# Performance work log

Measured on AMD Instinct MI355X. Metric: run time of the kernel, lower is better.

Reference implementation:

```python
import jax, jax.numpy as jnp
import numpy as np

B, L, D = 2, 2048, 2048
H, KVH = 16, 4
DK = D // H            # 128
REP = H // KVH         # 4
CAP = 50.0


def _rope(x):
    # x: [B, h, L, DK]; rotate-half style RoPE matching the torch module
    half = DK // 2
    inv_freq = 1.0 / (10000.0 ** (jnp.arange(0, DK, 2, dtype=jnp.float32) / DK))
    pos = jnp.arange(x.shape[2], dtype=jnp.float32)
    freqs = pos[:, None] * inv_freq[None, :]          # [L, DK/2]
    cos = jnp.cos(freqs).astype(x.dtype)
    sin = jnp.sin(freqs).astype(x.dtype)
    x1, x2 = x[..., :half], x[..., half:]
    return jnp.concatenate([x1 * cos - x2 * sin, x1 * sin + x2 * cos], axis=-1)


def setup_inputs() -> dict:
    key = jax.random.key(0)
    ks = jax.random.split(key, 7)
    query = jax.random.normal(ks[0], (B, L, D), jnp.float32)
    key_t = jax.random.normal(ks[1], (B, L, D), jnp.float32)
    value = jax.random.normal(ks[2], (B, L, D), jnp.float32)
    mask = jnp.tril(jnp.ones((L, L), dtype=bool))[None, None]  # causal, broadcast over B,H
    s = 1.0 / np.sqrt(D)
    Wq = jax.random.normal(ks[3], (D, D), jnp.float32) * s
    Wk = jax.random.normal(ks[4], (D // REP, D), jnp.float32) * s
    Wv = jax.random.normal(ks[5], (D // REP, D), jnp.float32) * s
    Wo = jax.random.normal(ks[6], (D, D), jnp.float32) * s
    return {"query": query, "key_t": key_t, "value": value, "mask": mask,
            "Wq": Wq, "Wk": Wk, "Wv": Wv, "Wo": Wo}


def reference(query, key_t, value, mask, Wq, Wk, Wv, Wo):
    Lk = key_t.shape[1]
    Q = (query @ Wq.T).reshape(B, L, H, DK).transpose(0, 2, 1, 3)        # [B,H,L,DK]
    K = (key_t @ Wk.T).reshape(B, Lk, KVH, DK).transpose(0, 2, 1, 3)     # [B,KVH,Lk,DK]
    V = (value @ Wv.T).reshape(B, Lk, KVH, DK).transpose(0, 2, 1, 3)
    # repeat_interleave KV heads to match query heads (GQA)
    K = jnp.repeat(K, REP, axis=1)
    V = jnp.repeat(V, REP, axis=1)
    Q = _rope(Q)
    K = _rope(K)
    # module implements "softcap" as a clamp on q/k pre-SDPA
    Q = jnp.clip(Q, -CAP, CAP)
    K = jnp.clip(K, -CAP, CAP)
    scale = 1.0 / np.sqrt(DK)  # SDPA default scaling
    logits = jnp.einsum('bhld,bhkd->bhlk', Q, K) * scale
    neg = jnp.finfo(logits.dtype).min
    logits = logits + jnp.where(mask, jnp.zeros((), logits.dtype), neg)
    attn = jax.nn.softmax(logits, axis=-1)
    out = jnp.einsum('bhlk,bhkd->bhld', attn, V)                         # [B,H,L,DK]
    out = out.transpose(0, 2, 1, 3).reshape(B, L, D)
    return out @ Wo.T
```

## Files before the change

### kernel.cpp

```cpp
#include <hip/hip_runtime.h>

typedef __bf16 bf16;
typedef __bf16 bf16x8 __attribute__((ext_vector_type(8)));
typedef float  f32x4  __attribute__((ext_vector_type(4)));

#define MFMA16(a, b, c) __builtin_amdgcn_mfma_f32_16x16x32_bf16((a), (b), (c), 0, 0, 0)

__device__ inline void gl_lds16(const bf16* g, bf16* l) {
  __builtin_amdgcn_global_load_lds(
      (const __attribute__((address_space(1))) void*)g,
      (__attribute__((address_space(3))) void*)l, 16, 0, 0);
}

__device__ inline bf16x8 cvt8(const float* __restrict__ f) {
  float4 a = *(const float4*)f;
  float4 b = *(const float4*)(f + 4);
  bf16x8 r;
  r[0] = (bf16)a.x; r[1] = (bf16)a.y; r[2] = (bf16)a.z; r[3] = (bf16)a.w;
  r[4] = (bf16)b.x; r[5] = (bf16)b.y; r[6] = (bf16)b.z; r[7] = (bf16)b.w;
  return r;
}

__global__ void cvt_f32_bf16(const float* __restrict__ src, bf16* __restrict__ dst,
                             int n8) {
  int i = blockIdx.x * 256 + threadIdx.x;
  if (i >= n8) return;
  *(bf16x8*)(dst + (size_t)i * 8) = cvt8(src + (size_t)i * 8);
}

__global__ __launch_bounds__(256) void gemm_qkv(const bf16* __restrict__ qA,
                                                const float* __restrict__ kA,
                                                const float* __restrict__ vA,
                                                const bf16* __restrict__ W,
                                                bf16* __restrict__ Qb,
                                                bf16* __restrict__ Kb,
                                                bf16* __restrict__ Vb) {
  __shared__ alignas(16) bf16 As[16 * 512];
  __shared__ alignas(16) bf16 Bs[16 * 512];

  const int tid  = threadIdx.x;
  const int wave = tid >> 6, lane = tid & 63;
  const int wm = wave >> 1, wn = wave & 1;
  const int lr = lane & 15, quad = lane >> 4;
  const int m0 = blockIdx.y * 128, n0 = blockIdx.x * 128;
  const int K = 2048;

  const int range = (n0 < 2048) ? 0 : (n0 < 2560) ? 1 : 2;
  const float* Af = (range == 1) ? kA : vA;

  f32x4 vzero = {0.f, 0.f, 0.f, 0.f};
  f32x4 acc[4][4];
#pragma unroll
  for (int mt = 0; mt < 4; ++mt)
#pragma unroll
    for (int nt = 0; nt < 4; ++nt) acc[mt][nt] = vzero;

  for (int k0 = 0; k0 < K; k0 += 64) {
#pragma unroll
    for (int j = 0; j < 4; ++j) {
      int c = wave * 4 + j;
      gl_lds16(W + (size_t)(n0 + (c >> 1) * 16 + lr) * K + k0 + (c & 1) * 32 + quad * 8,
               Bs + c * 512);
    }
    if (range == 0) {
#pragma unroll
      for (int j = 0; j < 4; ++j) {
        int c = wave * 4 + j;
        gl_lds16(qA + (size_t)(m0 + (c >> 1) * 16 + lr) * K +
                     k0 + (c & 1) * 32 + quad * 8,
                 As + c * 512);
      }
    } else {
#pragma unroll
      for (int j = 0; j < 4; ++j) {
        int c = wave * 4 + j;
        *(bf16x8*)(As + c * 512 + lane * 8) =
            cvt8(Af + (size_t)(m0 + (c >> 1) * 16 + lr) * K +
                 k0 + (c & 1) * 32 + quad * 8);
      }
    }
    __syncthreads();

#pragma unroll
    for (int s = 0; s < 2; ++s) {
      bf16x8 af[4], bfg[4];
#pragma unroll
      for (int mt = 0; mt < 4; ++mt)
        af[mt] = *(const bf16x8*)(As + ((wm * 4 + mt) * 2 + s) * 512 + lane * 8);
#pragma unroll
      for (int nt = 0; nt < 4; ++nt)
        bfg[nt] = *(const bf16x8*)(Bs + ((wn * 4 + nt) * 2 + s) * 512 + lane * 8);
#pragma unroll
      for (int mt = 0; mt < 4; ++mt)
#pragma unroll
        for (int nt = 0; nt < 4; ++nt)
          acc[mt][nt] = MFMA16(af[mt], bfg[nt], acc[mt][nt]);
    }
    __syncthreads();
  }

  bf16* Cb = (range == 0) ? Qb : (range == 1) ? Kb : Vb;
  const int ld = (range == 0) ? 2048 : 512;
  const int nb = (range == 0) ? n0 : (range == 1) ? n0 - 2048 : n0 - 2560;
#pragma unroll
  for (int mt = 0; mt < 4; ++mt) {
    int row = m0 + wm * 64 + mt * 16 + quad * 4;
#pragma unroll
    for (int nt = 0; nt < 4; ++nt) {
      int col = nb + wn * 64 + nt * 16 + lr;
#pragma unroll
      for (int e = 0; e < 4; ++e)
        Cb[(size_t)(row + e) * ld + col] = (bf16)acc[mt][nt][e];
    }
  }
}

template <bool OUTF32>
__global__ __launch_bounds__(256) void gemm_bt(const bf16* __restrict__ Ap,
                                               const bf16* __restrict__ W,
                                               void* __restrict__ C0,
                                               int ld0, int M, int N, int K) {
  __shared__ alignas(16) bf16 As[16 * 512];
  __shared__ alignas(16) bf16 Bs[16 * 512];

  const int tid  = threadIdx.x;
  const int wave = tid >> 6, lane = tid & 63;
  const int wm = wave >> 1, wn = wave & 1;
  const int lr = lane & 15, quad = lane >> 4;
  const int m0 = blockIdx.y * 128, n0 = blockIdx.x * 128;

  f32x4 vzero = {0.f, 0.f, 0.f, 0.f};
  f32x4 acc[4][4];
#pragma unroll
  for (int mt = 0; mt < 4; ++mt)
#pragma unroll
    for (int nt = 0; nt < 4; ++nt) acc[mt][nt] = vzero;

  for (int k0 = 0; k0 < K; k0 += 64) {
#pragma unroll
    for (int j = 0; j < 4; ++j) {
      int c = wave * 4 + j;
      gl_lds16(W + (size_t)(n0 + (c >> 1) * 16 + lr) * K + k0 + (c & 1) * 32 + quad * 8,
               Bs + c * 512);
      gl_lds16(Ap + (size_t)(m0 + (c >> 1) * 16 + lr) * K + k0 + (c & 1) * 32 + quad * 8,
               As + c * 512);
    }
    __syncthreads();

#pragma unroll
    for (int s = 0; s < 2; ++s) {
      bf16x8 af[4], bfg[4];
#pragma unroll
      for (int mt = 0; mt < 4; ++mt)
        af[mt] = *(const bf16x8*)(As + ((wm * 4 + mt) * 2 + s) * 512 + lane * 8);
#pragma unroll
      for (int nt = 0; nt < 4; ++nt)
        bfg[nt] = *(const bf16x8*)(Bs + ((wn * 4 + nt) * 2 + s) * 512 + lane * 8);
#pragma unroll
      for (int mt = 0; mt < 4; ++mt)
#pragma unroll
        for (int nt = 0; nt < 4; ++nt)
          acc[mt][nt] = MFMA16(af[mt], bfg[nt], acc[mt][nt]);
    }
    __syncthreads();
  }

#pragma unroll
  for (int mt = 0; mt < 4; ++mt) {
    int row = m0 + wm * 64 + mt * 16 + quad * 4;
#pragma unroll
    for (int nt = 0; nt < 4; ++nt) {
      int col = n0 + wn * 64 + nt * 16 + lr;
#pragma unroll
      for (int e = 0; e < 4; ++e) {
        if (OUTF32)
          ((float*)C0)[(size_t)(row + e) * ld0 + col] = acc[mt][nt][e];
        else
          ((bf16*)C0)[(size_t)(row + e) * ld0 + col] = (bf16)acc[mt][nt][e];
      }
    }
  }
}

__global__ void rope_clip(bf16* __restrict__ X, int heads, float scl) {
  int tpr = heads * 8;
  int idx = blockIdx.x * 256 + threadIdx.x;
  if (idx >= 4096 * tpr) return;
  int r = idx / tpr;
  int rem = idx - r * tpr;
  int h = rem >> 3, j0 = (rem & 7) * 8;
  int l = r & 2047;
  size_t base = (size_t)r * (heads * 128) + h * 128 + j0;
  bf16x8 x1 = *(const bf16x8*)(X + base);
  bf16x8 x2 = *(const bf16x8*)(X + base + 64);
  bf16x8 y1, y2;
#pragma unroll
  for (int t = 0; t < 8; ++t) {
    int j = j0 + t;
    float inv = expf(-(float)j * (9.210340371976184f / 64.0f));
    float s, c;
    sincosf((float)l * inv, &s, &c);
    float a = (float)x1[t], b = (float)x2[t];
    float u = a * c - b * s;
    float v = a * s + b * c;
    y1[t] = (bf16)(fminf(fmaxf(u, -50.f), 50.f) * scl);
    y2[t] = (bf16)(fminf(fmaxf(v, -50.f), 50.f) * scl);
  }
  *(bf16x8*)(X + base)      = y1;
  *(bf16x8*)(X + base + 64) = y2;
}

__global__ void transpose_bf16(const bf16* __restrict__ in, bf16* __restrict__ out,
                               int R, int Cc) {
  __shared__ bf16 t[32][33];
  int b = blockIdx.z;
  const bf16* ip = in + (size_t)b * R * Cc;
  bf16* op = out + (size_t)b * R * Cc;
  int c0 = blockIdx.x * 32, r0 = blockIdx.y * 32;
  int lx = threadIdx.x, ly = threadIdx.y;
#pragma unroll
  for (int i = 0; i < 32; i += 8)
    t[ly + i][lx] = ip[(size_t)(r0 + ly + i) * Cc + c0 + lx];
  __syncthreads();
#pragma unroll
  for (int i = 0; i < 32; i += 8)
    op[(size_t)(c0 + ly + i) * R + r0 + lx] = t[lx][ly + i];
}

__global__ __launch_bounds__(512, 2) void flash(const bf16* __restrict__ Q,
                                                const bf16* __restrict__ Kp,
                                                const bf16* __restrict__ Vt,
                                                bf16* __restrict__ Ctx) {
  __shared__ alignas(16) bf16 Ks[2][16 * 512];
  __shared__ alignas(16) bf16 Vs[2][16 * 512];
  __shared__ alignas(16) bf16 Ps[8][32 * 72];

  const int tid  = threadIdx.x;
  const int wave = tid >> 6, lane = tid & 63;
  const int lr = lane & 15, quad = lane >> 4;
  const int bh = blockIdx.y;
  const int b = bh >> 4, h = bh & 15, hk = h >> 2;
  const int p = blockIdx.x;
  const int qA0 = p * 128, qB0 = (15 - p) * 128;
  const int qbA = qA0 + wave * 16;
  const int qbB = qB0 + wave * 16;
  const int nt = (qB0 + 128) >> 6;

  bf16x8 qfA[4], qfB[4];
  {
    const bf16* qa = Q + ((size_t)(b * 2048 + qbA + lr)) * 2048 + h * 128 + quad * 8;
    const bf16* qbp = Q + ((size_t)(b * 2048 + qbB + lr)) * 2048 + h * 128 + quad * 8;
#pragma unroll
    for (int ks = 0; ks < 4; ++ks) {
      qfA[ks] = *(const bf16x8*)(qa + ks * 32);
      qfB[ks] = *(const bf16x8*)(qbp + ks * 32);
    }
  }

  f32x4 vzero = {0.f, 0.f, 0.f, 0.f};
  f32x4 oA[8], oB[8];
#pragma unroll
  for (int dt = 0; dt < 8; ++dt) { oA[dt] = vzero; oB[dt] = vzero; }
  float flsA[4] = {0.f, 0.f, 0.f, 0.f};
  float flsB[4] = {0.f, 0.f, 0.f, 0.f};

  const bf16* kbase = Kp + (size_t)(b * 2048) * 512 + hk * 128;
  const bf16* vbase = Vt + ((size_t)(b * 512 + hk * 128)) * 2048;

#define STAGE(bufi, kk)                                                         \
  do {                                                                          \
    _Pragma("unroll") for (int j = 0; j < 4; ++j) {                             \
      int c = wave * 4 + j;                                                     \
      if (c < 16) {                                                             \
        gl_lds16(kbase + (size_t)((kk) + (c >> 2) * 16 + lr) * 512 +            \
                     (c & 3) * 32 + quad * 8,                                   \
                 &Ks[bufi][c * 512]);                                           \
      } else {                                                                  \
        int c2 = c - 16;                                                        \
        gl_lds16(vbase + (size_t)((c2 >> 1) * 16 + lr) * 2048 + (kk) +          \
                     (c2 & 1) * 32 + quad * 8,                                  \
                 &Vs[bufi][c2 * 512]);                                          \
      }                                                                         \
    }                                                                           \
  } while (0)

  STAGE(0, 0);
  int cur = 0;

  for (int t = 0; t < nt; ++t) {
    const int k0 = t * 64;
    if (t + 1 < nt) {
      STAGE(cur ^ 1, k0 + 64);
      asm volatile("s_waitcnt vmcnt(4)" ::: "memory");
    } else {
      asm volatile("s_waitcnt vmcnt(0)" ::: "memory");
    }
    __builtin_amdgcn_s_barrier();

    const bf16* ksb = Ks[cur];
    const bf16* vsb = Vs[cur];

    if (k0 <= qbA + 15) {
      f32x4 sA[4], sB[4];
#pragma unroll
      for (int kt = 0; kt < 4; ++kt) { sA[kt] = vzero; sB[kt] = vzero; }
#pragma unroll
      for (int ks = 0; ks < 4; ++ks) {
#pragma unroll
        for (int kt = 0; kt < 4; ++kt) {
          bf16x8 kf = *(const bf16x8*)(ksb + (kt * 4 + ks) * 512 + lane * 8);
          sA[kt] = MFMA16(qfA[ks], kf, sA[kt]);
          sB[kt] = MFMA16(qfB[ks], kf, sB[kt]);
        }
      }
      bf16* pwA = Ps[wave];
      bf16* pwB = Ps[wave] + 16 * 72;
#pragma unroll
      for (int kt = 0; kt < 4; ++kt) {
        int kid = k0 + kt * 16 + lr;
#pragma unroll
        for (int e = 0; e < 4; ++e) {
          int qr = quad * 4 + e;
          float pa = (kid <= qbA + qr) ? __expf(sA[kt][e]) : 0.f;
          float pb = __expf(sB[kt][e]);
          flsA[e] += pa;
          flsB[e] += pb;
          pwA[qr * 72 + kt * 16 + lr] = (bf16)pa;
          pwB[qr * 72 + kt * 16 + lr] = (bf16)pb;
        }
      }
#pragma unroll
      for (int ks2 = 0; ks2 < 2; ++ks2) {
        bf16x8 pfA = *(const bf16x8*)(pwA + (size_t)lr * 72 + ks2 * 32 + quad * 8);
        bf16x8 pfB = *(const bf16x8*)(pwB + (size_t)lr * 72 + ks2 * 32 + quad * 8);
#pragma unroll
        for (int dt = 0; dt < 8; ++dt) {
          bf16x8 vf = *(const bf16x8*)(vsb + (dt * 2 + ks2) * 512 + lane * 8);
          oA[dt] = MFMA16(pfA, vf, oA[dt]);
          oB[dt] = MFMA16(pfB, vf, oB[dt]);
        }
      }
    } else if (k0 <= qbB + 15) {
      f32x4 s[4];
#pragma unroll
      for (int kt = 0; kt < 4; ++kt) s[kt] = vzero;
#pragma unroll
      for (int ks = 0; ks < 4; ++ks) {
#pragma unroll
        for (int kt = 0; kt < 4; ++kt) {
          bf16x8 kf = *(const bf16x8*)(ksb + (kt * 4 + ks) * 512 + lane * 8);
          s[kt] = MFMA16(qfB[ks], kf, s[kt]);
        }
      }
      bf16* pwB = Ps[wave] + 16 * 72;
#pragma unroll
      for (int kt = 0; kt < 4; ++kt) {
        int kid = k0 + kt * 16 + lr;
#pragma unroll
        for (int e = 0; e < 4; ++e) {
          int qr = quad * 4 + e;
          float pb = (kid <= qbB + qr) ? __expf(s[kt][e]) : 0.f;
          flsB[e] += pb;
          pwB[qr * 72 + kt * 16 + lr] = (bf16)pb;
        }
      }
#pragma unroll
      for (int ks2 = 0; ks2 < 2; ++ks2) {
        bf16x8 pf = *(const bf16x8*)(pwB + (size_t)lr * 72 + ks2 * 32 + quad * 8);
#pragma unroll
        for (int dt = 0; dt < 8; ++dt) {
          bf16x8 vf = *(const bf16x8*)(vsb + (dt * 2 + ks2) * 512 + lane * 8);
          oB[dt] = MFMA16(pf, vf, oB[dt]);
        }
      }
    }
    __builtin_amdgcn_s_barrier();
    cur ^= 1;
  }
#undef STAGE

#pragma unroll
  for (int e = 0; e < 4; ++e) {
    float sa = flsA[e];
    sa += __shfl_xor(sa, 1);
    sa += __shfl_xor(sa, 2);
    sa += __shfl_xor(sa, 4);
    sa += __shfl_xor(sa, 8);
    flsA[e] = 1.0f / sa;
    float sb = flsB[e];
    sb += __shfl_xor(sb, 1);
    sb += __shfl_xor(sb, 2);
    sb += __shfl_xor(sb, 4);
    sb += __shfl_xor(sb, 8);
    flsB[e] = 1.0f / sb;
  }

  bf16* ca = Ctx + ((size_t)(b * 2048 + qbA + quad * 4)) * 2048 + h * 128 + lr;
  bf16* cb = Ctx + ((size_t)(b * 2048 + qbB + quad * 4)) * 2048 + h * 128 + lr;
#pragma unroll
  for (int dt = 0; dt < 8; ++dt)
#pragma unroll
    for (int e = 0; e < 4; ++e) {
      ca[(size_t)e * 2048 + dt * 16] = (bf16)(oA[dt][e] * flsA[e]);
      cb[(size_t)e * 2048 + dt * 16] = (bf16)(oB[dt][e] * flsB[e]);
    }
}

extern "C" void kernel_launch(void* const* d_in, const int* in_sizes, int n_in,
                              void* d_out, int out_size, void* d_ws, size_t ws_size,
                              hipStream_t stream) {
  (void)in_sizes; (void)n_in; (void)out_size; (void)ws_size;
  const float* query = (const float*)d_in[0];
  const float* key_t = (const float*)d_in[1];
  const float* value = (const float*)d_in[2];
  const float* Wq = (const float*)d_in[4];
  const float* Wk = (const float*)d_in[5];
  const float* Wv = (const float*)d_in[6];
  const float* Wo = (const float*)d_in[7];

  const size_t MB = 1024ull * 1024ull;
  char* ws  = (char*)d_ws;
  bf16* qbf = (bf16*)(ws);
  bf16* wqb = (bf16*)(ws + 16 * MB);
  bf16* wkb = (bf16*)(ws + 24 * MB);
  bf16* wvb = (bf16*)(ws + 26 * MB);
  bf16* wob = (bf16*)(ws + 28 * MB);
  bf16* Qb  = (bf16*)(ws + 36 * MB);
  bf16* Kb  = (bf16*)(ws + 52 * MB);
  bf16* Vb  = (bf16*)(ws + 56 * MB);
  bf16* Vtb = (bf16*)(ws + 60 * MB);
  bf16* Ctx = qbf;

  cvt_f32_bf16<<<4096, 256, 0, stream>>>(query, qbf, 1048576);
  cvt_f32_bf16<<<2048, 256, 0, stream>>>(Wq, wqb, 524288);
  cvt_f32_bf16<<<512, 256, 0, stream>>>(Wk, wkb, 131072);
  cvt_f32_bf16<<<512, 256, 0, stream>>>(Wv, wvb, 131072);
  cvt_f32_bf16<<<2048, 256, 0, stream>>>(Wo, wob, 524288);

  gemm_qkv<<<dim3(24, 32), 256, 0, stream>>>(qbf, key_t, value, wqb, Qb, Kb, Vb);

  rope_clip<<<2048, 256, 0, stream>>>(Qb, 16, 0.08838834764831845f);
  rope_clip<<<512, 256, 0, stream>>>(Kb, 4, 1.0f);

  transpose_bf16<<<dim3(16, 64, 2), dim3(32, 8), 0, stream>>>(Vb, Vtb, 2048, 512);

  flash<<<dim3(8, 32), 512, 0, stream>>>(Qb, Kb, Vtb, Ctx);

  gemm_bt<true><<<dim3(16, 32), 256, 0, stream>>>(
      Ctx, wob, (float*)d_out, 2048, 4096, 2048, 2048);
}
```

Measured before the change: 471.1 us.

## Double-buffer LDS tiles in QKV and output GEMMs to overlap loads with MFMA

```diff
diff --git a/kernel.cpp b/kernel.cpp
--- a/kernel.cpp
+++ b/kernel.cpp
@@ -21,6 +21,13 @@
   return r;
 }
 
+__device__ inline bf16x8 cvt8v(float4 a, float4 b) {
+  bf16x8 r;
+  r[0] = (bf16)a.x; r[1] = (bf16)a.y; r[2] = (bf16)a.z; r[3] = (bf16)a.w;
+  r[4] = (bf16)b.x; r[5] = (bf16)b.y; r[6] = (bf16)b.z; r[7] = (bf16)b.w;
+  return r;
+}
+
 __global__ void cvt_f32_bf16(const float* __restrict__ src, bf16* __restrict__ dst,
                              int n8) {
   int i = blockIdx.x * 256 + threadIdx.x;
@@ -35,15 +42,15 @@
                                                 bf16* __restrict__ Qb,
                                                 bf16* __restrict__ Kb,
                                                 bf16* __restrict__ Vb) {
-  __shared__ alignas(16) bf16 As[16 * 512];
-  __shared__ alignas(16) bf16 Bs[16 * 512];
+  __shared__ alignas(16) bf16 As[2][16 * 512];
+  __shared__ alignas(16) bf16 Bs[2][16 * 512];
 
   const int tid  = threadIdx.x;
   const int wave = tid >> 6, lane = tid & 63;
   const int wm = wave >> 1, wn = wave & 1;
   const int lr = lane & 15, quad = lane >> 4;
   const int m0 = blockIdx.y * 128, n0 = blockIdx.x * 128;
-  const int K = 2048;
+  const int NS = 32;
 
   const int range = (n0 < 2048) ? 0 : (n0 < 2560) ? 1 : 2;
   const float* Af = (range == 1) ? kA : vA;
@@ -55,49 +62,118 @@
 #pragma unroll
     for (int nt = 0; nt < 4; ++nt) acc[mt][nt] = vzero;
 
-  for (int k0 = 0; k0 < K; k0 += 64) {
-#pragma unroll
-    for (int j = 0; j < 4; ++j) {
-      int c = wave * 4 + j;
-      gl_lds16(W + (size_t)(n0 + (c >> 1) * 16 + lr) * K + k0 + (c & 1) * 32 + quad * 8,
-               Bs + c * 512);
-    }
-    if (range == 0) {
-#pragma unroll
-      for (int j = 0; j < 4; ++j) {
-        int c = wave * 4 + j;
-        gl_lds16(qA + (size_t)(m0 + (c >> 1) * 16 + lr) * K +
-                     k0 + (c & 1) * 32 + quad * 8,
-                 As + c * 512);
-      }
-    } else {
-#pragma unroll
-      for (int j = 0; j < 4; ++j) {
-        int c = wave * 4 + j;
-        *(bf16x8*)(As + c * 512 + lane * 8) =
-            cvt8(Af + (size_t)(m0 + (c >> 1) * 16 + lr) * K +
-                 k0 + (c & 1) * 32 + quad * 8);
-      }
-    }
-    __syncthreads();
-
-#pragma unroll
-    for (int s = 0; s < 2; ++s) {
-      bf16x8 af[4], bfg[4];
-#pragma unroll
-      for (int mt = 0; mt < 4; ++mt)
-        af[mt] = *(const bf16x8*)(As + ((wm * 4 + mt) * 2 + s) * 512 + lane * 8);
-#pragma unroll
-      for (int nt = 0; nt < 4; ++nt)
-        bfg[nt] = *(const bf16x8*)(Bs + ((wn * 4 + nt) * 2 + s) * 512 + lane * 8);
-#pragma unroll
-      for (int mt = 0; mt < 4; ++mt)
-#pragma unroll
-        for (int nt = 0; nt < 4; ++nt)
-          acc[mt][nt] = MFMA16(af[mt], bfg[nt], acc[mt][nt]);
-    }
-    __syncthreads();
-  }
+#define BSTAGE(bufi, kk)                                                        \
+  do {                                                                          \
+    _Pragma("unroll") for (int j = 0; j < 4; ++j) {                             \
+      int c = wave * 4 + j;                                                     \
+      gl_lds16(W + (size_t)(n0 + (c >> 1) * 16 + lr) * 2048 + (kk) +            \
+                   (c & 1) * 32 + quad * 8,                                     \
+               &Bs[bufi][c * 512]);                                             \
+    }                                                                           \
+  } while (0)
+
+#define ABSTAGE(bufi, kk)                                                       \
+  do {                                                                          \
+    _Pragma("unroll") for (int j = 0; j < 4; ++j) {                             \
+      int c = wave * 4 + j;                                                     \
+      gl_lds16(qA + (size_t)(m0 + (c >> 1) * 16 + lr) * 2048 + (kk) +           \
+                   (c & 1) * 32 + quad * 8,                                     \
+               &As[bufi][c * 512]);                                             \
+    }                                                                           \
+  } while (0)
+
+#define AISSUE(kk, ar)                                                          \
+  do {                                                                          \
+    _Pragma("unroll") for (int j = 0; j < 4; ++j) {                             \
+      int c = wave * 4 + j;                                                     \
+      const float* ap_ = Af + (size_t)(m0 + (c >> 1) * 16 + lr) * 2048 + (kk) + \
+                         (c & 1) * 32 + quad * 8;                               \
+      ar[j * 2]     = *(const float4*)ap_;                                      \
+      ar[j * 2 + 1] = *(const float4*)(ap_ + 4);                                \
+    }                                                                           \
+  } while (0)
+
+#define AWRITE(bufi, ar)                                                        \
+  do {                                                                          \
+    _Pragma("unroll") for (int j = 0; j < 4; ++j) {                             \
+      int c = wave * 4 + j;                                                     \
+      *(bf16x8*)(&As[bufi][c * 512] + lane * 8) = cvt8v(ar[j * 2], ar[j * 2 + 1]); \
+    }                                                                           \
+  } while (0)
+
+#define QKV_COMPUTE(bufi)                                                       \
+  do {                                                                          \
+    _Pragma("unroll") for (int s = 0; s < 2; ++s) {                             \
+      bf16x8 af[4], bfg[4];                                                     \
+      _Pragma("unroll") for (int mt = 0; mt < 4; ++mt)                          \
+        af[mt] = *(const bf16x8*)(&As[bufi][((wm * 4 + mt) * 2 + s) * 512] +    \
+                                  lane * 8);                                    \
+      _Pragma("unroll") for (int nt = 0; nt < 4; ++nt)                          \
+        bfg[nt] = *(const bf16x8*)(&Bs[bufi][((wn * 4 + nt) * 2 + s) * 512] +   \
+                                   lane * 8);                                   \
+      _Pragma("unroll") for (int mt = 0; mt < 4; ++mt)                          \
+        _Pragma("unroll") for (int nt = 0; nt < 4; ++nt)                        \
+          acc[mt][nt] = MFMA16(af[mt], bfg[nt], acc[mt][nt]);                   \
+    }                                                                           \
+  } while (0)
+
+  if (range == 0) {
+    BSTAGE(0, 0);
+    ABSTAGE(0, 0);
+    int cur = 0;
+    for (int t = 0; t < NS; ++t) {
+      if (t + 1 < NS) {
+        BSTAGE(cur ^ 1, (t + 1) * 64);
+        ABSTAGE(cur ^ 1, (t + 1) * 64);
+        asm volatile("s_waitcnt vmcnt(8)" ::: "memory");
+      } else {
+        asm volatile("s_waitcnt vmcnt(0)" ::: "memory");
+      }
+      __builtin_amdgcn_s_barrier();
+      QKV_COMPUTE(cur);
+      __builtin_amdgcn_s_barrier();
+      cur ^= 1;
+    }
+  } else {
+    float4 arA[8], arB[8];
+    AISSUE(0, arA);
+    BSTAGE(0, 0);
+    AWRITE(0, arA);
+    int cur = 0;
+    for (int t = 0; t < NS; t += 2) {
+      if (t + 1 < NS) {
+        BSTAGE(cur ^ 1, (t + 1) * 64);
+        AISSUE((t + 1) * 64, arB);
+        asm volatile("s_waitcnt vmcnt(12)" ::: "memory");
+      } else {
+        asm volatile("s_waitcnt vmcnt(0)" ::: "memory");
+      }
+      asm volatile("s_waitcnt lgkmcnt(0)" ::: "memory");
+      __builtin_amdgcn_s_barrier();
+      QKV_COMPUTE(cur);
+      if (t + 1 < NS) AWRITE(cur ^ 1, arB);
+      __builtin_amdgcn_s_barrier();
+      cur ^= 1;
+      if (t + 2 < NS) {
+        BSTAGE(cur ^ 1, (t + 2) * 64);
+        AISSUE((t + 2) * 64, arA);
+        asm volatile("s_waitcnt vmcnt(12)" ::: "memory");
+      } else {
+        asm volatile("s_waitcnt vmcnt(0)" ::: "memory");
+      }
+      asm volatile("s_waitcnt lgkmcnt(0)" ::: "memory");
+      __builtin_amdgcn_s_barrier();
+      QKV_COMPUTE(cur);
+      if (t + 2 < NS) AWRITE(cur ^ 1, arA);
+      __builtin_amdgcn_s_barrier();
+      cur ^= 1;
+    }
+  }
+#undef BSTAGE
+#undef ABSTAGE
+#undef AISSUE
+#undef AWRITE
+#undef QKV_COMPUTE
 
   bf16* Cb = (range == 0) ? Qb : (range == 1) ? Kb : Vb;
   const int ld = (range == 0) ? 2048 : 512;
@@ -120,14 +196,15 @@
                                                const bf16* __restrict__ W,
                                                void* __restrict__ C0,
                                                int ld0, int M, int N, int K) {
-  __shared__ alignas(16) bf16 As[16 * 512];
-  __shared__ alignas(16) bf16 Bs[16 * 512];
+  __shared__ alignas(16) bf16 As[2][16 * 512];
+  __shared__ alignas(16) bf16 Bs[2][16 * 512];
 
   const int tid  = threadIdx.x;
   const int wave = tid >> 6, lane = tid & 63;
   const int wm = wave >> 1, wn = wave & 1;
   const int lr = lane & 15, quad = lane >> 4;
   const int m0 = blockIdx.y * 128, n0 = blockIdx.x * 128;
+  const int NS = K >> 6;
 
   f32x4 vzero = {0.f, 0.f, 0.f, 0.f};
   f32x4 acc[4][4];
@@ -136,34 +213,48 @@
 #pragma unroll
     for (int nt = 0; nt < 4; ++nt) acc[mt][nt] = vzero;
 
-  for (int k0 = 0; k0 < K; k0 += 64) {
-#pragma unroll
-    for (int j = 0; j < 4; ++j) {
-      int c = wave * 4 + j;
-      gl_lds16(W + (size_t)(n0 + (c >> 1) * 16 + lr) * K + k0 + (c & 1) * 32 + quad * 8,
-               Bs + c * 512);
-      gl_lds16(Ap + (size_t)(m0 + (c >> 1) * 16 + lr) * K + k0 + (c & 1) * 32 + quad * 8,
-               As + c * 512);
-    }
-    __syncthreads();
-
+#define STAGE8(bufi, kk)                                                        \
+  do {                                                                          \
+    _Pragma("unroll") for (int j = 0; j < 4; ++j) {                             \
+      int c = wave * 4 + j;                                                     \
+      gl_lds16(W + (size_t)(n0 + (c >> 1) * 16 + lr) * K + (kk) +               \
+                   (c & 1) * 32 + quad * 8,                                     \
+               &Bs[bufi][c * 512]);                                             \
+      gl_lds16(Ap + (size_t)(m0 + (c >> 1) * 16 + lr) * K + (kk) +              \
+                   (c & 1) * 32 + quad * 8,                                     \
+               &As[bufi][c * 512]);                                             \
+    }                                                                           \
+  } while (0)
+
+  STAGE8(0, 0);
+  int cur = 0;
+  for (int t = 0; t < NS; ++t) {
+    if (t + 1 < NS) {
+      STAGE8(cur ^ 1, (t + 1) * 64);
+      asm volatile("s_waitcnt vmcnt(8)" ::: "memory");
+    } else {
+      asm volatile("s_waitcnt vmcnt(0)" ::: "memory");
+    }
+    __builtin_amdgcn_s_barrier();
 #pragma unroll
     for (int s = 0; s < 2; ++s) {
       bf16x8 af[4], bfg[4];
 #pragma unroll
       for (int mt = 0; mt < 4; ++mt)
-        af[mt] = *(const bf16x8*)(As + ((wm * 4 + mt) * 2 + s) * 512 + lane * 8);
+        af[mt] = *(const bf16x8*)(&As[cur][((wm * 4 + mt) * 2 + s) * 512] + lane * 8);
 #pragma unroll
       for (int nt = 0; nt < 4; ++nt)
-        bfg[nt] = *(const bf16x8*)(Bs + ((wn * 4 + nt) * 2 + s) * 512 + lane * 8);
+        bfg[nt] = *(const bf16x8*)(&Bs[cur][((wn * 4 + nt) * 2 + s) * 512] + lane * 8);
 #pragma unroll
       for (int mt = 0; mt < 4; ++mt)
 #pragma unroll
         for (int nt = 0; nt < 4; ++nt)
           acc[mt][nt] = MFMA16(af[mt], bfg[nt], acc[mt][nt]);
     }
-    __syncthreads();
-  }
+    __builtin_amdgcn_s_barrier();
+    cur ^= 1;
+  }
+#undef STAGE8
 
 #pragma unroll
   for (int mt = 0; mt < 4; ++mt) {
```

After: 470.4 us. Within noise of the previous version (-0.1%).

## Double-buffer GEMMs, use 256x256 QKV tile, pre-convert K/V inputs to bf16

Applied to the files above, without the earlier changes.

```diff
diff --git a/kernel.cpp b/kernel.cpp
--- a/kernel.cpp
+++ b/kernel.cpp
@@ -28,25 +28,145 @@
   *(bf16x8*)(dst + (size_t)i * 8) = cvt8(src + (size_t)i * 8);
 }
 
-__global__ __launch_bounds__(256) void gemm_qkv(const bf16* __restrict__ qA,
-                                                const float* __restrict__ kA,
-                                                const float* __restrict__ vA,
-                                                const bf16* __restrict__ W,
-                                                bf16* __restrict__ Qb,
-                                                bf16* __restrict__ Kb,
-                                                bf16* __restrict__ Vb) {
-  __shared__ alignas(16) bf16 As[16 * 512];
-  __shared__ alignas(16) bf16 Bs[16 * 512];
+__global__ __launch_bounds__(512, 2) void gemm_qkv256(const bf16* __restrict__ qA,
+                                                      const bf16* __restrict__ kA,
+                                                      const bf16* __restrict__ vA,
+                                                      const bf16* __restrict__ W,
+                                                      bf16* __restrict__ Qb,
+                                                      bf16* __restrict__ Kb,
+                                                      bf16* __restrict__ Vb) {
+  __shared__ alignas(16) bf16 As[2][32 * 512];
+  __shared__ alignas(16) bf16 Bs[2][32 * 512];
+
+  const int tid  = threadIdx.x;
+  const int wave = tid >> 6, lane = tid & 63;
+  const int wm = wave >> 2, wn = wave & 3;
+  const int lr = lane & 15, quad = lane >> 4;
+  const int n0 = blockIdx.x * 256, m0 = blockIdx.y * 256;
+  const int NS = 32;
+
+  const int range = (n0 < 2048) ? 0 : (n0 < 2560) ? 1 : 2;
+  const bf16* Ab = (range == 0) ? qA : (range == 1) ? kA : vA;
+
+  f32x4 vzero = {0.f, 0.f, 0.f, 0.f};
+  f32x4 acc[8][4];
+#pragma unroll
+  for (int mt = 0; mt < 8; ++mt)
+#pragma unroll
+    for (int nt = 0; nt < 4; ++nt) acc[mt][nt] = vzero;
+
+#define STAGE256(bufi, kk)                                                      \
+  do {                                                                          \
+    _Pragma("unroll") for (int j = 0; j < 4; ++j) {                             \
+      int c = wave * 4 + j;                                                     \
+      int mi = c >> 1, sl = c & 1;                                              \
+      gl_lds16(Ab + (size_t)(m0 + mi * 16 + lr) * 2048 + (kk) + sl * 32 + quad * 8, \
+               &As[bufi][c * 512]);                                             \
+      gl_lds16(W + (size_t)(n0 + mi * 16 + lr) * 2048 + (kk) + sl * 32 + quad * 8,  \
+               &Bs[bufi][c * 512]);                                             \
+    }                                                                           \
+  } while (0)
+
+  STAGE256(0, 0);
+  int cur = 0;
+  for (int t = 0; t < NS; ++t) {
+    if (t + 1 < NS) {
+      STAGE256(cur ^ 1, (t + 1) * 64);
+      asm volatile("s_waitcnt vmcnt(8)" ::: "memory");
+    } else {
+      asm volatile("s_waitcnt vmcnt(0)" ::: "memory");
+    }
+    __builtin_amdgcn_s_barrier();
+
+    const bf16* as = As[cur];
+    const bf16* bs = Bs[cur];
+    bf16x8 af[4], bf0[4], bf1[4];
+
+#pragma unroll
+    for (int nt = 0; nt < 4; ++nt)
+      bf0[nt] = *(const bf16x8*)(bs + ((wn * 4 + nt) * 2 + 0) * 512 + lane * 8);
+#pragma unroll
+    for (int mt = 0; mt < 4; ++mt)
+      af[mt] = *(const bf16x8*)(as + ((wm * 8 + mt) * 2 + 0) * 512 + lane * 8);
+    __builtin_amdgcn_s_setprio(1);
+#pragma unroll
+    for (int mt = 0; mt < 4; ++mt)
+#pragma unroll
+      for (int nt = 0; nt < 4; ++nt)
+        acc[mt][nt] = MFMA16(af[mt], bf0[nt], acc[mt][nt]);
+    __builtin_amdgcn_s_setprio(0);
+
+#pragma unroll
+    for (int mt = 0; mt < 4; ++mt)
+      af[mt] = *(const bf16x8*)(as + ((wm * 8 + 4 + mt) * 2 + 0) * 512 + lane * 8);
+    __builtin_amdgcn_s_setprio(1);
+#pragma unroll
+    for (int mt = 0; mt < 4; ++mt)
+#pragma unroll
+      for (int nt = 0; nt < 4; ++nt)
+        acc[4 + mt][nt] = MFMA16(af[mt], bf0[nt], acc[4 + mt][nt]);
+    __builtin_amdgcn_s_setprio(0);
+
+#pragma unroll
+    for (int nt = 0; nt < 4; ++nt)
+      bf1[nt] = *(const bf16x8*)(bs + ((wn * 4 + nt) * 2 + 1) * 512 + lane * 8);
+#pragma unroll
+    for (int mt = 0; mt < 4; ++mt)
+      af[mt] = *(const bf16x8*)(as + ((wm * 8 + mt) * 2 + 1) * 512 + lane * 8);
+    __builtin_amdgcn_s_setprio(1);
+#pragma unroll
+    for (int mt = 0; mt < 4; ++mt)
+#pragma unroll
+      for (int nt = 0; nt < 4; ++nt)
+        acc[mt][nt] = MFMA16(af[mt], bf1[nt], acc[mt][nt]);
+    __builtin_amdgcn_s_setprio(0);
+
+#pragma unroll
+    for (int mt = 0; mt < 4; ++mt)
+      af[mt] = *(const bf16x8*)(as + ((wm * 8 + 4 + mt) * 2 + 1) * 512 + lane * 8);
+    __builtin_amdgcn_s_setprio(1);
+#pragma unroll
+    for (int mt = 0; mt < 4; ++mt)
+#pragma unroll
+      for (int nt = 0; nt < 4; ++nt)
+        acc[4 + mt][nt] = MFMA16(af[mt], bf1[nt], acc[4 + mt][nt]);
+    __builtin_amdgcn_s_setprio(0);
+
+    __builtin_amdgcn_s_barrier();
+    cur ^= 1;
+  }
+#undef STAGE256
+
+  bf16* Cb = (range == 0) ? Qb : (range == 1) ? Kb : Vb;
+  const int ld = (range == 0) ? 2048 : 512;
+  const int nb = (range == 0) ? n0 : (range == 1) ? n0 - 2048 : n0 - 2560;
+#pragma unroll
+  for (int mt = 0; mt < 8; ++mt) {
+    int row = m0 + wm * 128 + mt * 16 + quad * 4;
+#pragma unroll
+    for (int nt = 0; nt < 4; ++nt) {
+      int col = nb + wn * 64 + nt * 16 + lr;
+#pragma unroll
+      for (int e = 0; e < 4; ++e)
+        Cb[(size_t)(row + e) * ld + col] = (bf16)acc[mt][nt][e];
+    }
+  }
+}
+
+template <bool OUTF32>
+__global__ __launch_bounds__(256) void gemm_bt(const bf16* __restrict__ Ap,
+                                               const bf16* __restrict__ W,
+                                               void* __restrict__ C0,
+                                               int ld0, int M, int N, int K) {
+  __shared__ alignas(16) bf16 As[2][16 * 512];
+  __shared__ alignas(16) bf16 Bs[2][16 * 512];
 
   const int tid  = threadIdx.x;
   const int wave = tid >> 6, lane = tid & 63;
   const int wm = wave >> 1, wn = wave & 1;
   const int lr = lane & 15, quad = lane >> 4;
   const int m0 = blockIdx.y * 128, n0 = blockIdx.x * 128;
-  const int K = 2048;
-
-  const int range = (n0 < 2048) ? 0 : (n0 < 2560) ? 1 : 2;
-  const float* Af = (range == 1) ? kA : vA;
+  const int NS = K >> 6;
 
   f32x4 vzero = {0.f, 0.f, 0.f, 0.f};
   f32x4 acc[4][4];
@@ -55,115 +175,50 @@
 #pragma unroll
     for (int nt = 0; nt < 4; ++nt) acc[mt][nt] = vzero;
 
-  for (int k0 = 0; k0 < K; k0 += 64) {
-#pragma unroll
-    for (int j = 0; j < 4; ++j) {
-      int c = wave * 4 + j;
-      gl_lds16(W + (size_t)(n0 + (c >> 1) * 16 + lr) * K + k0 + (c & 1) * 32 + quad * 8,
-               Bs + c * 512);
-    }
-    if (range == 0) {
-#pragma unroll
-      for (int j = 0; j < 4; ++j) {
-        int c = wave * 4 + j;
-        gl_lds16(qA + (size_t)(m0 + (c >> 1) * 16 + lr) * K +
-                     k0 + (c & 1) * 32 + quad * 8,
-                 As + c * 512);
-      }
+#define STAGE8(bufi, kk)                                                        \
+  do {                                                                          \
+    _Pragma("unroll") for (int j = 0; j < 4; ++j) {                             \
+      int c = wave * 4 + j;                                                     \
+      gl_lds16(W + (size_t)(n0 + (c >> 1) * 16 + lr) * K + (kk) +               \
+                   (c & 1) * 32 + quad * 8,                                     \
+               &Bs[bufi][c * 512]);                                             \
+      gl_lds16(Ap + (size_t)(m0 + (c >> 1) * 16 + lr) * K + (kk) +              \
+                   (c & 1) * 32 + quad * 8,                                     \
+               &As[bufi][c * 512]);                                             \
+    }                                                                           \
+  } while (0)
+
+  STAGE8(0, 0);
+  int cur = 0;
+  for (int t = 0; t < NS; ++t) {
+    if (t + 1 < NS) {
+      STAGE8(cur ^ 1, (t + 1) * 64);
+      asm volatile("s_waitcnt vmcnt(8)" ::: "memory");
     } else {
-#pragma unroll
-      for (int j = 0; j < 4; ++j) {
-        int c = wave * 4 + j;
-        *(bf16x8*)(As + c * 512 + lane * 8) =
-            cvt8(Af + (size_t)(m0 + (c >> 1) * 16 + lr) * K +
-                 k0 + (c & 1) * 32 + quad * 8);
-      }
-    }
-    __syncthreads();
-
+      asm volatile("s_waitcnt vmcnt(0)" ::: "memory");
+    }
+    __builtin_amdgcn_s_barrier();
 #pragma unroll
     for (int s = 0; s < 2; ++s) {
       bf16x8 af[4], bfg[4];
 #pragma unroll
       for (int mt = 0; mt < 4; ++mt)
-        af[mt] = *(const bf16x8*)(As + ((wm * 4 + mt) * 2 + s) * 512 + lane * 8);
+        af[mt] = *(const bf16x8*)(&As[cur][((wm * 4 + mt) * 2 + s) * 512] + lane * 8);
 #pragma unroll
       for (int nt = 0; nt < 4; ++nt)
-        bfg[nt] = *(const bf16x8*)(Bs + ((wn * 4 + nt) * 2 + s) * 512 + lane * 8);
+        bfg[nt] = *(const bf16x8*)(&Bs[cur][((wn * 4 + nt) * 2 + s) * 512] + lane * 8);
+      __builtin_amdgcn_s_setprio(1);
 #pragma unroll
       for (int mt = 0; mt < 4; ++mt)
 #pragma unroll
         for (int nt = 0; nt < 4; ++nt)
           acc[mt][nt] = MFMA16(af[mt], bfg[nt], acc[mt][nt]);
-    }
-    __syncthreads();
-  }
-
-  bf16* Cb = (range == 0) ? Qb : (range == 1) ? Kb : Vb;
-  const int ld = (range == 0) ? 2048 : 512;
-  const int nb = (range == 0) ? n0 : (range == 1) ? n0 - 2048 : n0 - 2560;
-#pragma unroll
-  for (int mt = 0; mt < 4; ++mt) {
-    int row = m0 + wm * 64 + mt * 16 + quad * 4;
-#pragma unroll
-    for (int nt = 0; nt < 4; ++nt) {
-      int col = nb + wn * 64 + nt * 16 + lr;
-#pragma unroll
-      for (int e = 0; e < 4; ++e)
-        Cb[(size_t)(row + e) * ld + col] = (bf16)acc[mt][nt][e];
-    }
-  }
-}
-
-template <bool OUTF32>
-__global__ __launch_bounds__(256) void gemm_bt(const bf16* __restrict__ Ap,
-                                               const bf16* __restrict__ W,
-                                               void* __restrict__ C0,
-                                               int ld0, int M, int N, int K) {
-  __shared__ alignas(16) bf16 As[16 * 512];
-  __shared__ alignas(16) bf16 Bs[16 * 512];
-
-  const int tid  = threadIdx.x;
-  const int wave = tid >> 6, lane = tid & 63;
-  const int wm = wave >> 1, wn = wave & 1;
-  const int lr = lane & 15, quad = lane >> 4;
-  const int m0 = blockIdx.y * 128, n0 = blockIdx.x * 128;
-
-  f32x4 vzero = {0.f, 0.f, 0.f, 0.f};
-  f32x4 acc[4][4];
-#pragma unroll
-  for (int mt = 0; mt < 4; ++mt)
-#pragma unroll
-    for (int nt = 0; nt < 4; ++nt) acc[mt][nt] = vzero;
-
-  for (int k0 = 0; k0 < K; k0 += 64) {
-#pragma unroll
-    for (int j = 0; j < 4; ++j) {
-      int c = wave * 4 + j;
-      gl_lds16(W + (size_t)(n0 + (c >> 1) * 16 + lr) * K + k0 + (c & 1) * 32 + quad * 8,
-               Bs + c * 512);
-      gl_lds16(Ap + (size_t)(m0 + (c >> 1) * 16 + lr) * K + k0 + (c & 1) * 32 + quad * 8,
-               As + c * 512);
-    }
-    __syncthreads();
-
-#pragma unroll
-    for (int s = 0; s < 2; ++s) {
-      bf16x8 af[4], bfg[4];
-#pragma unroll
-      for (int mt = 0; mt < 4; ++mt)
-        af[mt] = *(const bf16x8*)(As + ((wm * 4 + mt) * 2 + s) * 512 + lane * 8);
-#pragma unroll
-      for (int nt = 0; nt < 4; ++nt)
-        bfg[nt] = *(const bf16x8*)(Bs + ((wn * 4 + nt) * 2 + s) * 512 + lane * 8);
-#pragma unroll
-      for (int mt = 0; mt < 4; ++mt)
-#pragma unroll
-        for (int nt = 0; nt < 4; ++nt)
-          acc[mt][nt] = MFMA16(af[mt], bfg[nt], acc[mt][nt]);
-    }
-    __syncthreads();
-  }
+      __builtin_amdgcn_s_setprio(0);
+    }
+    __builtin_amdgcn_s_barrier();
+    cur ^= 1;
+  }
+#undef STAGE8
 
 #pragma unroll
   for (int mt = 0; mt < 4; ++mt) {
@@ -429,15 +484,19 @@
   bf16* Kb  = (bf16*)(ws + 52 * MB);
   bf16* Vb  = (bf16*)(ws + 56 * MB);
   bf16* Vtb = (bf16*)(ws + 60 * MB);
+  bf16* kb16 = (bf16*)(ws + 64 * MB);
+  bf16* vb16 = (bf16*)(ws + 80 * MB);
   bf16* Ctx = qbf;
 
   cvt_f32_bf16<<<4096, 256, 0, stream>>>(query, qbf, 1048576);
+  cvt_f32_bf16<<<4096, 256, 0, stream>>>(key_t, kb16, 1048576);
+  cvt_f32_bf16<<<4096, 256, 0, stream>>>(value, vb16, 1048576);
   cvt_f32_bf16<<<2048, 256, 0, stream>>>(Wq, wqb, 524288);
   cvt_f32_bf16<<<512, 256, 0, stream>>>(Wk, wkb, 131072);
   cvt_f32_bf16<<<512, 256, 0, stream>>>(Wv, wvb, 131072);
   cvt_f32_bf16<<<2048, 256, 0, stream>>>(Wo, wob, 524288);
 
-  gemm_qkv<<<dim3(24, 32), 256, 0, stream>>>(qbf, key_t, value, wqb, Qb, Kb, Vb);
+  gemm_qkv256<<<dim3(12, 16), 512, 0, stream>>>(qbf, kb16, vb16, wqb, Qb, Kb, Vb);
 
   rope_clip<<<2048, 256, 0, stream>>>(Qb, 16, 0.08838834764831845f);
   rope_clip<<<512, 256, 0, stream>>>(Kb, 4, 1.0f);
```

After: 431.5 us. 8.4% less time.
